# Performance work log

Measured on AMD Instinct MI355X. Metric: run time of the kernel, lower is better.

The kernel has to match this reference:

```python
import jax, jax.numpy as jnp
import numpy as np

B, T, C, H = 4, 2048, 1024, 16
D = C // H          # head dim = 64
W_FF = 4 * C        # 4096
EPS = 1e-5


def layernorm(x, w, b):
    mu = jnp.mean(x, axis=-1, keepdims=True)
    var = jnp.mean(jnp.square(x - mu), axis=-1, keepdims=True)
    return (x - mu) / jnp.sqrt(var + EPS) * w + b


def setup_inputs() -> dict:
    key = jax.random.key(0)
    ks = jax.random.split(key, 12)
    s_attn = 1.0 / np.sqrt(C)
    s_ff1 = 1.0 / np.sqrt(C)
    s_ff2 = 1.0 / np.sqrt(W_FF)
    return {
        "x": jax.random.normal(ks[0], (B, T, C), jnp.float32),
        "ln1_w": jnp.ones((C,), jnp.float32),
        "ln1_b": jnp.zeros((C,), jnp.float32),
        # weights stored [in, out] (transpose of torch Linear.weight)
        "Wq": jax.random.normal(ks[1], (C, C), jnp.float32) * s_attn,
        "bq": jnp.zeros((C,), jnp.float32),
        "Wk": jax.random.normal(ks[2], (C, C), jnp.float32) * s_attn,
        "bk": jnp.zeros((C,), jnp.float32),
        "Wv": jax.random.normal(ks[3], (C, C), jnp.float32) * s_attn,
        "bv": jnp.zeros((C,), jnp.float32),
        "Wo": jax.random.normal(ks[4], (C, C), jnp.float32) * s_attn,
        "bo": jnp.zeros((C,), jnp.float32),
        "ln2_w": jnp.ones((C,), jnp.float32),
        "ln2_b": jnp.zeros((C,), jnp.float32),
        "W1": jax.random.normal(ks[5], (C, W_FF), jnp.float32) * s_ff1,
        "b1": jnp.zeros((W_FF,), jnp.float32),
        "W2": jax.random.normal(ks[6], (W_FF, C), jnp.float32) * s_ff2,
        "b2": jnp.zeros((C,), jnp.float32),
    }


def reference(x, ln1_w, ln1_b, Wq, bq, Wk, bk, Wv, bv, Wo, bo,
              ln2_w, ln2_b, W1, b1, W2, b2):
    b, t, c = x.shape
    # --- attention branch ---
    h = layernorm(x, ln1_w, ln1_b)
    q = (h @ Wq + bq).reshape(b, t, H, D)
    k = (h @ Wk + bk).reshape(b, t, H, D)
    v = (h @ Wv + bv).reshape(b, t, H, D)
    att = jnp.einsum("bqhd,bkhd->bhqk", q, k) / jnp.sqrt(jnp.float32(D))
    causal = jnp.tril(jnp.ones((t, t), bool))
    att = jnp.where(causal, att, -jnp.inf)
    p = jax.nn.softmax(att, axis=-1)
    y = jnp.einsum("bhqk,bkhd->bqhd", p, v).reshape(b, t, c)
    x = x + y @ Wo + bo
    # --- MLP branch (depth=2: one hidden relu layer) ---
    h2 = layernorm(x, ln2_w, ln2_b)
    x = x + jax.nn.relu(h2 @ W1 + b1) @ W2 + b2
    return x
```

## Files before the change

kernel.cpp:

```cpp
#include <hip/hip_runtime.h>
#include <cstdint>
#include <cstddef>

typedef unsigned short u16;
typedef __attribute__((ext_vector_type(8))) short bf16x8;
typedef __attribute__((ext_vector_type(4))) float f32x4;
typedef __attribute__((ext_vector_type(16))) float f32x16;
typedef __attribute__((ext_vector_type(4))) unsigned short u16x4;

#define DEV static __device__ __forceinline__

DEV u16 f2bf(float f) {
  union { float f; uint32_t u; } c; c.f = f;
  uint32_t u = c.u;
  return (u16)((u + 0x7fffu + ((u >> 16) & 1u)) >> 16);
}

DEV void gload16(const void* g, void* l) {
  __builtin_amdgcn_global_load_lds((const __attribute__((address_space(1))) void*)g,
                                   (__attribute__((address_space(3))) void*)l, 16, 0, 0);
}

__global__ __launch_bounds__(256)
void wconv_kernel(const float* __restrict__ W, u16* __restrict__ Wt, int K, int N) {
  __shared__ float tile[32][33];
  const int k0 = blockIdx.y << 5;
  const int n0 = blockIdx.x << 5;
  const int c  = threadIdx.x & 31;
  const int r0 = threadIdx.x >> 5;
#pragma unroll
  for (int i = 0; i < 4; i++) {
    int r = r0 + i * 8;
    tile[r][c] = W[(size_t)(k0 + r) * N + n0 + c];
  }
  __syncthreads();
#pragma unroll
  for (int i = 0; i < 4; i++) {
    int r = r0 + i * 8;
    Wt[(size_t)(n0 + r) * K + k0 + c] = f2bf(tile[c][r]);
  }
}

__global__ void bcat_kernel(const float* __restrict__ bq, const float* __restrict__ bk,
                            const float* __restrict__ bv, float* __restrict__ o) {
  int i = blockIdx.x * 256 + threadIdx.x;
  float v = (i < 1024) ? bq[i] : (i < 2048 ? bk[i - 1024] : bv[i - 2048]);
  o[i] = v;
}

__global__ __launch_bounds__(256)
void ln_kernel(const float* __restrict__ x, const float* __restrict__ w,
               const float* __restrict__ b, u16* __restrict__ out) {
  const int row = blockIdx.x;
  const int t = threadIdx.x;
  __shared__ float red[4];
  const float4 v = ((const float4*)(x + (size_t)row * 1024))[t];
  float s = v.x + v.y + v.z + v.w;
#pragma unroll
  for (int off = 32; off; off >>= 1) s += __shfl_xor(s, off);
  if ((t & 63) == 0) red[t >> 6] = s;
  __syncthreads();
  const float mu = (red[0] + red[1] + red[2] + red[3]) * (1.0f / 1024.0f);
  __syncthreads();
  float dx = v.x - mu, dy = v.y - mu, dz = v.z - mu, dw = v.w - mu;
  float ss = dx * dx + dy * dy + dz * dz + dw * dw;
#pragma unroll
  for (int off = 32; off; off >>= 1) ss += __shfl_xor(ss, off);
  if ((t & 63) == 0) red[t >> 6] = ss;
  __syncthreads();
  const float var = (red[0] + red[1] + red[2] + red[3]) * (1.0f / 1024.0f);
  const float rstd = rsqrtf(var + 1e-5f);
  const float4 wv = ((const float4*)w)[t];
  const float4 bv = ((const float4*)b)[t];
  u16x4 o;
  o[0] = f2bf(dx * rstd * wv.x + bv.x);
  o[1] = f2bf(dy * rstd * wv.y + bv.y);
  o[2] = f2bf(dz * rstd * wv.z + bv.z);
  o[3] = f2bf(dw * rstd * wv.w + bv.w);
  *((u16x4*)(out + (size_t)row * 1024 + t * 4)) = o;
}

template <bool RELU, bool RESID>
__global__ __launch_bounds__(256, 2)
void gemm_kernel(const u16* __restrict__ A, const u16* __restrict__ Bt,
                 const float* __restrict__ bias, const float* __restrict__ resid,
                 u16* __restrict__ outb, float* __restrict__ outf,
                 int M, int N, int K) {
  __shared__ short As[128 * 64];
  __shared__ short Bs[128 * 64];
  const int l = threadIdx.x & 63;
  const int w = threadIdx.x >> 6;
  const int m0 = blockIdx.y * 128;
  const int n0 = blockIdx.x * 128;
  const int mw = (w >> 1) * 64;
  const int nw = (w & 1) * 64;

  f32x4 acc[4][4];
#pragma unroll
  for (int i = 0; i < 4; i++)
#pragma unroll
    for (int j = 0; j < 4; j++) acc[i][j] = {0.f, 0.f, 0.f, 0.f};

  const int nk = K >> 6;
  for (int kt = 0; kt < nk; ++kt) {
    const int k0 = kt << 6;
#pragma unroll
    for (int i = 0; i < 4; i++) {
      int o = ((w * 4 + i) << 10) + l * 16;
      int row = o >> 7;
      int ke = (o & 127) >> 1;
      gload16(A + (size_t)(m0 + row) * K + k0 + ke, (short*)As + ((w * 4 + i) << 9));
      gload16(Bt + (size_t)(n0 + row) * K + k0 + ke, (short*)Bs + ((w * 4 + i) << 9));
    }
    __syncthreads();
#pragma unroll
    for (int kg = 0; kg < 2; ++kg) {
      bf16x8 af[4], bfr[4];
#pragma unroll
      for (int i = 0; i < 4; i++) {
        af[i]  = *(const bf16x8*)(As + (mw + i * 16 + (l & 15)) * 64 + kg * 32 + (l >> 4) * 8);
        bfr[i] = *(const bf16x8*)(Bs + (nw + i * 16 + (l & 15)) * 64 + kg * 32 + (l >> 4) * 8);
      }
#pragma unroll
      for (int i = 0; i < 4; i++)
#pragma unroll
        for (int j = 0; j < 4; j++)
          acc[i][j] = __builtin_amdgcn_mfma_f32_16x16x32_bf16(af[i], bfr[j], acc[i][j], 0, 0, 0);
    }
    __syncthreads();
  }

#pragma unroll
  for (int i = 0; i < 4; i++) {
    const int r0 = m0 + mw + i * 16 + ((l >> 4) << 2);
#pragma unroll
    for (int j = 0; j < 4; j++) {
      const int c = n0 + nw + j * 16 + (l & 15);
      const float bb = bias[c];
#pragma unroll
      for (int r = 0; r < 4; r++) {
        float v = acc[i][j][r] + bb;
        if (RELU) v = fmaxf(v, 0.0f);
        const size_t idx = (size_t)(r0 + r) * N + c;
        if (RESID)
          outf[idx] = resid[idx] + v;
        else
          outb[idx] = f2bf(v);
      }
    }
  }
}

__global__ __launch_bounds__(256)
void vtrans_kernel(const u16* __restrict__ QKV, u16* __restrict__ Vt_g) {
  __shared__ u16 tile[32][33];
  const int t0 = blockIdx.x * 32;
  const int d0 = blockIdx.y * 32;
  const int bh = blockIdx.z;
  const int bb = bh >> 4, hh = bh & 15;
  const int c = threadIdx.x & 31, r0 = threadIdx.x >> 5;
#pragma unroll
  for (int i = 0; i < 4; i++) {
    int r = r0 + i * 8;
    tile[r][c] = QKV[(size_t)(bb * 2048 + t0 + r) * 3072 + 2048 + hh * 64 + d0 + c];
  }
  __syncthreads();
#pragma unroll
  for (int i = 0; i < 4; i++) {
    int r = r0 + i * 8;
    Vt_g[((size_t)bh * 64 + d0 + r) * 2048 + t0 + c] = tile[c][r];
  }
}

__global__ __launch_bounds__(256, 3)
void attn_kernel(const u16* __restrict__ QKV, const u16* __restrict__ Vt_g,
                 u16* __restrict__ Y) {
  __shared__ short Ks[2][64 * 64];
  __shared__ short Vs[2][64 * 64];
  const int tid = threadIdx.x;
  const int l = tid & 63;
  const int w = tid >> 6;
  const int lane31 = l & 31;
  const int khalf = l >> 5;
  const int qt = gridDim.x - 1 - blockIdx.x;
  const int bh = blockIdx.y;
  const int bb = bh >> 4, hh = bh & 15;
  const size_t baseT = (size_t)bb * 2048;
  const int qrel = qt * 128 + w * 32 + lane31;
  const size_t qrow = baseT + qrel;
  const float SC = 0.125f * 1.44269504088896340736f;

  bf16x8 qf[4];
  {
    const u16* qp = QKV + qrow * 3072 + hh * 64 + khalf * 8;
#pragma unroll
    for (int s = 0; s < 4; s++) qf[s] = *(const bf16x8*)(qp + s * 16);
  }

  f32x16 yac0, yac1;
#pragma unroll
  for (int i = 0; i < 16; i++) { yac0[i] = 0.f; yac1[i] = 0.f; }
  float m_ = -INFINITY, s_ = 0.f;

  auto stage = [&](int j, int buf) {
    const u16* kb = QKV + (baseT + j * 64) * 3072 + 1024 + hh * 64;
    const u16* vb = Vt_g + (size_t)bh * 64 * 2048 + j * 64;
#pragma unroll
    for (int i = 0; i < 2; i++) {
      int idx = i * 256 + tid;
      int row = idx >> 3, cb = idx & 7;
      int cbs = (cb ^ (row & 7)) * 8;
      gload16(kb + (size_t)row * 3072 + cbs, &Ks[buf][(i * 256 + w * 64) * 8]);
      gload16(vb + (size_t)row * 2048 + cbs, &Vs[buf][(i * 256 + w * 64) * 8]);
    }
  };

  const int jmax = qt * 2 + 1;
  stage(0, 0);
  __syncthreads();
  int cur = 0;
  for (int j = 0; j <= jmax; ++j) {
    if (j < jmax) stage(j + 1, cur ^ 1);
    const short* Kc = Ks[cur];
    const short* Vc = Vs[cur];

    f32x16 sa0, sa1;
#pragma unroll
    for (int i = 0; i < 16; i++) { sa0[i] = 0.f; sa1[i] = 0.f; }
#pragma unroll
    for (int s = 0; s < 4; s++) {
      int cb = ((s * 2 + khalf) ^ (l & 7)) * 8;
      bf16x8 k0 = *(const bf16x8*)(Kc + lane31 * 64 + cb);
      bf16x8 k1 = *(const bf16x8*)(Kc + (32 + lane31) * 64 + cb);
      sa0 = __builtin_amdgcn_mfma_f32_32x32x16_bf16(k0, qf[s], sa0, 0, 0, 0);
      sa1 = __builtin_amdgcn_mfma_f32_32x32x16_bf16(k1, qf[s], sa1, 0, 0, 0);
    }

    float p0[16], p1[16];
    float tmax = -INFINITY;
    const int kb0 = j * 64 + 4 * khalf;
    const bool bnd = (j * 64 + 63) > (qt * 128 + w * 32);
#pragma unroll
    for (int r = 0; r < 16; r++) {
      float v0 = sa0[r] * SC, v1 = sa1[r] * SC;
      if (bnd) {
        int kg = kb0 + (r & 3) + 8 * (r >> 2);
        if (kg > qrel) v0 = -INFINITY;
        if (kg + 32 > qrel) v1 = -INFINITY;
      }
      p0[r] = v0; p1[r] = v1;
      tmax = fmaxf(tmax, fmaxf(v0, v1));
    }
    tmax = fmaxf(tmax, __shfl_xor(tmax, 32));
    const float nm = fmaxf(m_, tmax);
    const float alpha = exp2f(m_ - nm);
    m_ = nm;
    float sum = 0.f;
#pragma unroll
    for (int r = 0; r < 16; r++) {
      p0[r] = exp2f(p0[r] - nm);
      p1[r] = exp2f(p1[r] - nm);
      sum += p0[r] + p1[r];
    }
    sum += __shfl_xor(sum, 32);
    s_ = s_ * alpha + sum;
#pragma unroll
    for (int i = 0; i < 16; i++) { yac0[i] *= alpha; yac1[i] *= alpha; }

    uint32_t pk0[8], pk1[8];
#pragma unroll
    for (int jj = 0; jj < 4; jj++) {
      int rb = 4 * jj;
      uint32_t a, b;
      asm("v_cvt_pk_bf16_f32 %0, %1, %2" : "=v"(a) : "v"(p0[rb]), "v"(p0[rb + 1]));
      asm("v_cvt_pk_bf16_f32 %0, %1, %2" : "=v"(b) : "v"(p0[rb + 2]), "v"(p0[rb + 3]));
      pk0[jj] = a; pk1[jj] = b;
    }
#pragma unroll
    for (int jj = 0; jj < 4; jj++) {
      int rb = 4 * jj;
      uint32_t a, b;
      asm("v_cvt_pk_bf16_f32 %0, %1, %2" : "=v"(a) : "v"(p1[rb]), "v"(p1[rb + 1]));
      asm("v_cvt_pk_bf16_f32 %0, %1, %2" : "=v"(b) : "v"(p1[rb + 2]), "v"(p1[rb + 3]));
      pk0[4 + jj] = a; pk1[4 + jj] = b;
    }

#pragma unroll
    for (int kvs = 0; kvs < 4; kvs++) {
      uint32_t x0 = pk0[2 * kvs], y0 = pk0[2 * kvs + 1];
      uint32_t x1 = pk1[2 * kvs], y1 = pk1[2 * kvs + 1];
      asm volatile("v_permlane32_swap_b32 %0, %1" : "+v"(x0), "+v"(y0));
      asm volatile("v_permlane32_swap_b32 %0, %1" : "+v"(x1), "+v"(y1));
      union { uint32_t u[4]; bf16x8 v; } pf;
      pf.u[0] = x0; pf.u[1] = x1; pf.u[2] = y0; pf.u[3] = y1;
      int cb = ((kvs * 2 + khalf) ^ (l & 7)) * 8;
      bf16x8 v0 = *(const bf16x8*)(Vc + lane31 * 64 + cb);
      bf16x8 v1 = *(const bf16x8*)(Vc + (32 + lane31) * 64 + cb);
      yac0 = __builtin_amdgcn_mfma_f32_32x32x16_bf16(v0, pf.v, yac0, 0, 0, 0);
      yac1 = __builtin_amdgcn_mfma_f32_32x32x16_bf16(v1, pf.v, yac1, 0, 0, 0);
    }
    __syncthreads();
    cur ^= 1;
  }

  const float sinv = 1.0f / s_;
  u16* yp = Y + qrow * 1024 + hh * 64;
#pragma unroll
  for (int rq = 0; rq < 4; rq++) {
    u16x4 o0, o1;
#pragma unroll
    for (int e = 0; e < 4; e++) {
      o0[e] = f2bf(yac0[rq * 4 + e] * sinv);
      o1[e] = f2bf(yac1[rq * 4 + e] * sinv);
    }
    *(u16x4*)(yp + 8 * rq + 4 * khalf) = o0;
    *(u16x4*)(yp + 32 + 8 * rq + 4 * khalf) = o1;
  }
}

extern "C" void kernel_launch(void* const* d_in, const int* in_sizes, int n_in,
                              void* d_out, int out_size, void* d_ws, size_t ws_size,
                              hipStream_t stream) {
  const float* x    = (const float*)d_in[0];
  const float* ln1w = (const float*)d_in[1];
  const float* ln1b = (const float*)d_in[2];
  const float* Wq   = (const float*)d_in[3];
  const float* bq   = (const float*)d_in[4];
  const float* Wk   = (const float*)d_in[5];
  const float* bk   = (const float*)d_in[6];
  const float* Wv   = (const float*)d_in[7];
  const float* bv   = (const float*)d_in[8];
  const float* Wo   = (const float*)d_in[9];
  const float* bo   = (const float*)d_in[10];
  const float* ln2w = (const float*)d_in[11];
  const float* ln2b = (const float*)d_in[12];
  const float* W1   = (const float*)d_in[13];
  const float* b1   = (const float*)d_in[14];
  const float* W2   = (const float*)d_in[15];
  const float* b2   = (const float*)d_in[16];
  float* out = (float*)d_out;
  char* ws = (char*)d_ws;
  const size_t MB = 1ull << 20;

  u16* h     = (u16*)(ws);
  u16* qkv   = (u16*)(ws + 16 * MB);
  u16* ff1   = (u16*)(ws);
  u16* Vt_g  = (u16*)(ws + 64 * MB);
  float* x1  = (float*)(ws + 64 * MB);
  u16* y     = (u16*)(ws + 96 * MB);
  u16* Wqkvt = (u16*)(ws + 112 * MB);
  u16* Wot   = (u16*)(ws + 118 * MB);
  u16* W1t   = (u16*)(ws + 120 * MB);
  u16* W2t   = (u16*)(ws + 128 * MB);
  float* bqkv = (float*)(ws + 136 * MB);

  dim3 tb(256);
  wconv_kernel<<<dim3(32, 32), tb, 0, stream>>>(Wq, Wqkvt, 1024, 1024);
  wconv_kernel<<<dim3(32, 32), tb, 0, stream>>>(Wk, Wqkvt + (1024u * 1024), 1024, 1024);
  wconv_kernel<<<dim3(32, 32), tb, 0, stream>>>(Wv, Wqkvt + (2048u * 1024), 1024, 1024);
  wconv_kernel<<<dim3(32, 32), tb, 0, stream>>>(Wo, Wot, 1024, 1024);
  wconv_kernel<<<dim3(128, 32), tb, 0, stream>>>(W1, W1t, 1024, 4096);
  wconv_kernel<<<dim3(32, 128), tb, 0, stream>>>(W2, W2t, 4096, 1024);
  bcat_kernel<<<dim3(12), tb, 0, stream>>>(bq, bk, bv, bqkv);

  ln_kernel<<<8192, tb, 0, stream>>>(x, ln1w, ln1b, h);

  gemm_kernel<false, false><<<dim3(24, 64), tb, 0, stream>>>(h, Wqkvt, bqkv, nullptr, qkv, nullptr, 8192, 3072, 1024);

  vtrans_kernel<<<dim3(64, 2, 64), tb, 0, stream>>>(qkv, Vt_g);

  attn_kernel<<<dim3(16, 64), tb, 0, stream>>>(qkv, Vt_g, y);

  gemm_kernel<false, true><<<dim3(8, 64), tb, 0, stream>>>(y, Wot, bo, x, nullptr, x1, 8192, 1024, 1024);

  ln_kernel<<<8192, tb, 0, stream>>>(x1, ln2w, ln2b, y);

  gemm_kernel<true, false><<<dim3(32, 64), tb, 0, stream>>>(y, W1t, b1, nullptr, ff1, nullptr, 8192, 4096, 1024);

  gemm_kernel<false, true><<<dim3(8, 64), tb, 0, stream>>>(ff1, W2t, b2, x1, nullptr, out, 8192, 1024, 4096);
}
```

Before: 597.1 us.

## Shrink attention blocks to 64 queries, fold softmax scale into Wq, lazy rescale

The attention kernel now uses 2 waves (64 query rows) per block with twice as many blocks, so the causal triangle is split more finely and the load is better balanced. The 1/sqrt(D)*log2e scale is folded into Wq and bq during weight conversion, which removes a per-score multiply. The online softmax skips the rescale of the accumulator unless the running max grows by more than 8 (in log2 units), and MFMA sections are wrapped in s_setprio. Risks: the smaller blocks load each K/V tile for fewer queries, and the lazy rescale lets exponentials grow up to 2^8 in the bf16 P values.

Measured after the change: 622.7 us. +4.3%, slower.

```diff
diff --git a/kernel.cpp b/kernel.cpp
--- a/kernel.cpp
+++ b/kernel.cpp
@@ -22,7 +22,8 @@
 }
 
 __global__ __launch_bounds__(256)
-void wconv_kernel(const float* __restrict__ W, u16* __restrict__ Wt, int K, int N) {
+void wconv_kernel(const float* __restrict__ W, u16* __restrict__ Wt, int K, int N,
+                  float scale) {
   __shared__ float tile[32][33];
   const int k0 = blockIdx.y << 5;
   const int n0 = blockIdx.x << 5;
@@ -37,14 +38,15 @@
 #pragma unroll
   for (int i = 0; i < 4; i++) {
     int r = r0 + i * 8;
-    Wt[(size_t)(n0 + r) * K + k0 + c] = f2bf(tile[c][r]);
+    Wt[(size_t)(n0 + r) * K + k0 + c] = f2bf(tile[c][r] * scale);
   }
 }
 
 __global__ void bcat_kernel(const float* __restrict__ bq, const float* __restrict__ bk,
-                            const float* __restrict__ bv, float* __restrict__ o) {
+                            const float* __restrict__ bv, float* __restrict__ o,
+                            float sc) {
   int i = blockIdx.x * 256 + threadIdx.x;
-  float v = (i < 1024) ? bq[i] : (i < 2048 ? bk[i - 1024] : bv[i - 2048]);
+  float v = (i < 1024) ? bq[i] * sc : (i < 2048 ? bk[i - 1024] : bv[i - 2048]);
   o[i] = v;
 }
 
@@ -172,7 +174,7 @@
   }
 }
 
-__global__ __launch_bounds__(256, 3)
+__global__ __launch_bounds__(128, 2)
 void attn_kernel(const u16* __restrict__ QKV, const u16* __restrict__ Vt_g,
                  u16* __restrict__ Y) {
   __shared__ short Ks[2][64 * 64];
@@ -186,9 +188,8 @@
   const int bh = blockIdx.y;
   const int bb = bh >> 4, hh = bh & 15;
   const size_t baseT = (size_t)bb * 2048;
-  const int qrel = qt * 128 + w * 32 + lane31;
+  const int qrel = qt * 64 + w * 32 + lane31;
   const size_t qrow = baseT + qrel;
-  const float SC = 0.125f * 1.44269504088896340736f;
 
   bf16x8 qf[4];
   {
@@ -206,16 +207,16 @@
     const u16* kb = QKV + (baseT + j * 64) * 3072 + 1024 + hh * 64;
     const u16* vb = Vt_g + (size_t)bh * 64 * 2048 + j * 64;
 #pragma unroll
-    for (int i = 0; i < 2; i++) {
-      int idx = i * 256 + tid;
+    for (int i = 0; i < 4; i++) {
+      int idx = i * 128 + tid;
       int row = idx >> 3, cb = idx & 7;
       int cbs = (cb ^ (row & 7)) * 8;
-      gload16(kb + (size_t)row * 3072 + cbs, &Ks[buf][(i * 256 + w * 64) * 8]);
-      gload16(vb + (size_t)row * 2048 + cbs, &Vs[buf][(i * 256 + w * 64) * 8]);
+      gload16(kb + (size_t)row * 3072 + cbs, &Ks[buf][(i * 128 + w * 64) * 8]);
+      gload16(vb + (size_t)row * 2048 + cbs, &Vs[buf][(i * 128 + w * 64) * 8]);
     }
   };
 
-  const int jmax = qt * 2 + 1;
+  const int jmax = qt;
   stage(0, 0);
   __syncthreads();
   int cur = 0;
@@ -227,6 +228,7 @@
     f32x16 sa0, sa1;
 #pragma unroll
     for (int i = 0; i < 16; i++) { sa0[i] = 0.f; sa1[i] = 0.f; }
+    __builtin_amdgcn_s_setprio(1);
 #pragma unroll
     for (int s = 0; s < 4; s++) {
       int cb = ((s * 2 + khalf) ^ (l & 7)) * 8;
@@ -235,16 +237,16 @@
       sa0 = __builtin_amdgcn_mfma_f32_32x32x16_bf16(k0, qf[s], sa0, 0, 0, 0);
       sa1 = __builtin_amdgcn_mfma_f32_32x32x16_bf16(k1, qf[s], sa1, 0, 0, 0);
     }
+    __builtin_amdgcn_s_setprio(0);
 
     float p0[16], p1[16];
     float tmax = -INFINITY;
-    const int kb0 = j * 64 + 4 * khalf;
-    const bool bnd = (j * 64 + 63) > (qt * 128 + w * 32);
+    const bool bnd = (j == qt);
 #pragma unroll
     for (int r = 0; r < 16; r++) {
-      float v0 = sa0[r] * SC, v1 = sa1[r] * SC;
+      float v0 = sa0[r], v1 = sa1[r];
       if (bnd) {
-        int kg = kb0 + (r & 3) + 8 * (r >> 2);
+        int kg = j * 64 + 4 * khalf + (r & 3) + 8 * (r >> 2);
         if (kg > qrel) v0 = -INFINITY;
         if (kg + 32 > qrel) v1 = -INFINITY;
       }
@@ -252,20 +254,23 @@
       tmax = fmaxf(tmax, fmaxf(v0, v1));
     }
     tmax = fmaxf(tmax, __shfl_xor(tmax, 32));
-    const float nm = fmaxf(m_, tmax);
-    const float alpha = exp2f(m_ - nm);
-    m_ = nm;
+    if (!__all(tmax - m_ <= 8.0f)) {
+      const float nm = fmaxf(m_, tmax);
+      const float alpha = exp2f(m_ - nm);
+      m_ = nm;
+      s_ *= alpha;
+#pragma unroll
+      for (int i = 0; i < 16; i++) { yac0[i] *= alpha; yac1[i] *= alpha; }
+    }
     float sum = 0.f;
 #pragma unroll
     for (int r = 0; r < 16; r++) {
-      p0[r] = exp2f(p0[r] - nm);
-      p1[r] = exp2f(p1[r] - nm);
+      p0[r] = exp2f(p0[r] - m_);
+      p1[r] = exp2f(p1[r] - m_);
       sum += p0[r] + p1[r];
     }
     sum += __shfl_xor(sum, 32);
-    s_ = s_ * alpha + sum;
-#pragma unroll
-    for (int i = 0; i < 16; i++) { yac0[i] *= alpha; yac1[i] *= alpha; }
+    s_ += sum;
 
     uint32_t pk0[8], pk1[8];
 #pragma unroll
@@ -296,8 +301,10 @@
       int cb = ((kvs * 2 + khalf) ^ (l & 7)) * 8;
       bf16x8 v0 = *(const bf16x8*)(Vc + lane31 * 64 + cb);
       bf16x8 v1 = *(const bf16x8*)(Vc + (32 + lane31) * 64 + cb);
+      __builtin_amdgcn_s_setprio(1);
       yac0 = __builtin_amdgcn_mfma_f32_32x32x16_bf16(v0, pf.v, yac0, 0, 0, 0);
       yac1 = __builtin_amdgcn_mfma_f32_32x32x16_bf16(v1, pf.v, yac1, 0, 0, 0);
+      __builtin_amdgcn_s_setprio(0);
     }
     __syncthreads();
     cur ^= 1;
@@ -341,6 +348,7 @@
   float* out = (float*)d_out;
   char* ws = (char*)d_ws;
   const size_t MB = 1ull << 20;
+  const float SC = 0.125f * 1.44269504088896340736f;
 
   u16* h     = (u16*)(ws);
   u16* qkv   = (u16*)(ws + 16 * MB);
@@ -355,13 +363,13 @@
   float* bqkv = (float*)(ws + 136 * MB);
 
   dim3 tb(256);
-  wconv_kernel<<<dim3(32, 32), tb, 0, stream>>>(Wq, Wqkvt, 1024, 1024);
-  wconv_kernel<<<dim3(32, 32), tb, 0, stream>>>(Wk, Wqkvt + (1024u * 1024), 1024, 1024);
-  wconv_kernel<<<dim3(32, 32), tb, 0, stream>>>(Wv, Wqkvt + (2048u * 1024), 1024, 1024);
-  wconv_kernel<<<dim3(32, 32), tb, 0, stream>>>(Wo, Wot, 1024, 1024);
-  wconv_kernel<<<dim3(128, 32), tb, 0, stream>>>(W1, W1t, 1024, 4096);
-  wconv_kernel<<<dim3(32, 128), tb, 0, stream>>>(W2, W2t, 4096, 1024);
-  bcat_kernel<<<dim3(12), tb, 0, stream>>>(bq, bk, bv, bqkv);
+  wconv_kernel<<<dim3(32, 32), tb, 0, stream>>>(Wq, Wqkvt, 1024, 1024, SC);
+  wconv_kernel<<<dim3(32, 32), tb, 0, stream>>>(Wk, Wqkvt + (1024u * 1024), 1024, 1024, 1.0f);
+  wconv_kernel<<<dim3(32, 32), tb, 0, stream>>>(Wv, Wqkvt + (2048u * 1024), 1024, 1024, 1.0f);
+  wconv_kernel<<<dim3(32, 32), tb, 0, stream>>>(Wo, Wot, 1024, 1024, 1.0f);
+  wconv_kernel<<<dim3(128, 32), tb, 0, stream>>>(W1, W1t, 1024, 4096, 1.0f);
+  wconv_kernel<<<dim3(32, 128), tb, 0, stream>>>(W2, W2t, 4096, 1024, 1.0f);
+  bcat_kernel<<<dim3(12), tb, 0, stream>>>(bq, bk, bv, bqkv, SC);
 
   ln_kernel<<<8192, tb, 0, stream>>>(x, ln1w, ln1b, h);
 
@@ -369,7 +377,7 @@
 
   vtrans_kernel<<<dim3(64, 2, 64), tb, 0, stream>>>(qkv, Vt_g);
 
-  attn_kernel<<<dim3(16, 64), tb, 0, stream>>>(qkv, Vt_g, y);
+  attn_kernel<<<dim3(32, 64), dim3(128), 0, stream>>>(qkv, Vt_g, y);
 
   gemm_kernel<false, true><<<dim3(8, 64), tb, 0, stream>>>(y, Wot, bo, x, nullptr, x1, 8192, 1024, 1024);
 
```
